# Kernel tuning notes

Measured on AMD Instinct MI355X. Metric: run time of the kernel, lower is better.

The kernel has to match this reference:

```python
import jax, jax.numpy as jnp
import numpy as np

B, Ci, Cr, Hb, Wb = 2, 256, 128, 200, 200
Ca, NH, DH = 128, 8, 16          # attn_channels = min(256,128); 8 heads of dim 16
K = 100                           # max(16, int(0.5*W)), K < W so topk path is active
EPS = 1e-5


def ln(x, g, b):
    m = x.mean(-1, keepdims=True)
    v = ((x - m) ** 2).mean(-1, keepdims=True)
    return (x - m) / jnp.sqrt(v + EPS) * g + b


def setup_inputs() -> dict:
    key = jax.random.key(0)
    ks = jax.random.split(key, 16)
    def n(k, shape, s=0.02):
        return jax.random.normal(k, shape, dtype=jnp.float32) * s
    return dict(
        radar_features=jax.random.normal(ks[0], (B, Cr, Hb, Wb), dtype=jnp.float32),
        image_features=jax.random.normal(ks[1], (B, Ci, Hb, Wb), dtype=jnp.float32),
        img_proj_w=n(ks[2], (Ca, Ci)),
        rad_proj_w=n(ks[3], (Ca, Cr)),
        in_proj_w=n(ks[4], (3 * Ca, Ca)),
        in_proj_b=jnp.zeros((3 * Ca,), jnp.float32),
        out_proj_w=n(ks[5], (Ca, Ca)),
        out_proj_b=jnp.zeros((Ca,), jnp.float32),
        ln1q_g=jnp.ones((Ca,), jnp.float32), ln1q_b=jnp.zeros((Ca,), jnp.float32),
        ln1kv_g=jnp.ones((Ca,), jnp.float32), ln1kv_b=jnp.zeros((Ca,), jnp.float32),
        ln2_g=jnp.ones((Ca,), jnp.float32), ln2_b=jnp.zeros((Ca,), jnp.float32),
        ffn_w1=n(ks[6], (4 * Ca, Ca)), ffn_b1=jnp.zeros((4 * Ca,), jnp.float32),
        ffn_w2=n(ks[7], (Ca, 4 * Ca)), ffn_b2=jnp.zeros((Ca,), jnp.float32),
        score_w1=n(ks[8], (Ca // 2, 2 * Ca)), score_b1=jnp.zeros((Ca // 2,), jnp.float32),
        score_w2=n(ks[9], (1, Ca // 2)), score_b2=jnp.zeros((1,), jnp.float32),
        rad_delta_w=n(ks[10], (Cr, Ca)),
        gamma=jnp.full((1,), 0.5, jnp.float32),  # torch inits to 0; 0.5 so attn branch affects output
        gate_w=n(ks[11], (Cr, Cr + Ci)), gate_b=jnp.zeros((Cr,), jnp.float32),
        fuse_w=n(ks[12], (Cr + Ci, Cr + Ci, 3, 3)),
        bn_g=jnp.ones((Cr + Ci,), jnp.float32), bn_b=jnp.zeros((Cr + Ci,), jnp.float32),
    )


def reference(radar_features, image_features, img_proj_w, rad_proj_w, in_proj_w, in_proj_b,
              out_proj_w, out_proj_b, ln1q_g, ln1q_b, ln1kv_g, ln1kv_b, ln2_g, ln2_b,
              ffn_w1, ffn_b1, ffn_w2, ffn_b2, score_w1, score_b1, score_w2, score_b2,
              rad_delta_w, gamma, gate_w, gate_b, fuse_w, bn_g, bn_b):
    # 1x1 projections into attention space, then per-row sequences [B*H, W, Ca]
    img_seq = jnp.einsum('bchw,oc->bhwo', image_features, img_proj_w).reshape(B * Hb, Wb, Ca)
    rad_seq = jnp.einsum('bchw,oc->bhwo', radar_features, rad_proj_w).reshape(B * Hb, Wb, Ca)

    # progressive focus: score each image token per row, keep top-K as KV
    si = jnp.concatenate([jax.lax.stop_gradient(rad_seq), img_seq], axis=-1)
    h = jax.nn.relu(si @ score_w1.T + score_b1)
    score = (h @ score_w2.T + score_b2)[..., 0]            # [B*H, W]
    _, idx = jax.lax.top_k(score, K)                       # [B*H, K]
    img_kv = jnp.take_along_axis(img_seq, idx[:, :, None], axis=1)  # [B*H, K, Ca]

    # cross attention (pre-LN on q and kv, residual onto rad_seq)
    q = ln(rad_seq, ln1q_g, ln1q_b)
    kv = ln(img_kv, ln1kv_g, ln1kv_b)
    wq, wk, wv = in_proj_w[:Ca], in_proj_w[Ca:2 * Ca], in_proj_w[2 * Ca:]
    bq, bk, bv = in_proj_b[:Ca], in_proj_b[Ca:2 * Ca], in_proj_b[2 * Ca:]
    qh = (q @ wq.T + bq).reshape(B * Hb, Wb, NH, DH)
    kh = (kv @ wk.T + bk).reshape(B * Hb, K, NH, DH)
    vh = (kv @ wv.T + bv).reshape(B * Hb, K, NH, DH)
    att = jax.nn.softmax(jnp.einsum('nqhd,nkhd->nhqk', qh, kh) / jnp.sqrt(jnp.float32(DH)), axis=-1)
    o = jnp.einsum('nhqk,nkhd->nqhd', att, vh).reshape(B * Hb, Wb, Ca) @ out_proj_w.T + out_proj_b
    x = rad_seq + o
    x = x + (jax.nn.relu(ln(x, ln2_g, ln2_b) @ ffn_w1.T + ffn_b1) @ ffn_w2.T + ffn_b2)

    # back to BEV, project delta to radar channels
    delta = jnp.einsum('bhwc,oc->bohw', x.reshape(B, Hb, Wb, Ca), rad_delta_w)

    # cross-modal gate (1x1 conv + sigmoid) with range-decay mask
    gate_in = jnp.concatenate([radar_features, image_features], axis=1)
    gate = jax.nn.sigmoid(jnp.einsum('bchw,oc->bohw', gate_in, gate_w) + gate_b[None, :, None, None])
    y = jnp.arange(Hb, dtype=jnp.float32) / (Hb - 1)
    rmask = jnp.clip(1.0 - 0.7 * y, 0.3, None)[None, None, :, None]
    gate = gate * rmask

    radar_enhanced = radar_features + gamma * gate * delta

    # fuse: 3x3 conv + BatchNorm (batch stats, training mode) + ReLU
    fi = jnp.concatenate([radar_enhanced, image_features], axis=1)
    c = jax.lax.conv_general_dilated(fi, fuse_w, (1, 1), 'SAME',
                                     dimension_numbers=('NCHW', 'OIHW', 'NCHW'))
    m = c.mean((0, 2, 3), keepdims=True)
    v = ((c - m) ** 2).mean((0, 2, 3), keepdims=True)
    out = jax.nn.relu((c - m) / jnp.sqrt(v + EPS) * bn_g[None, :, None, None] + bn_b[None, :, None, None])
    return out
```

## Files before the change

kernel.cpp:

```cpp
#include <hip/hip_runtime.h>
#include <hip/hip_bf16.h>

#define EPSF 1e-5f

typedef unsigned short u16;
typedef unsigned int u32;
typedef __attribute__((ext_vector_type(8))) short short8v;
typedef __attribute__((ext_vector_type(4))) float f32x4;

__device__ float g_arena[84000000];
__device__ float g_stats[768];

__device__ __forceinline__ float wave_sum(float v) {
#pragma unroll
    for (int o = 32; o > 0; o >>= 1) v += __shfl_down(v, o, 64);
    return v;
}

__device__ __forceinline__ void gload16(const u16* g, u16* l) {
    __builtin_amdgcn_global_load_lds(
        (const __attribute__((address_space(1))) u32*)(g),
        (__attribute__((address_space(3))) u32*)(l),
        16, 0, 0);
}

__device__ __forceinline__ void bf_split(float v, u16& h, u16& l) {
    __hip_bfloat16 bh = __float2bfloat16(v);
    float hv = __bfloat162float(bh);
    __hip_bfloat16 bl = __float2bfloat16(v - hv);
    h = *reinterpret_cast<u16*>(&bh);
    l = *reinterpret_cast<u16*>(&bl);
}

__device__ __forceinline__ void store_bf4(u16* p, float4 v) {
    __hip_bfloat16 h0 = __float2bfloat16(v.x);
    __hip_bfloat16 h1 = __float2bfloat16(v.y);
    __hip_bfloat16 h2 = __float2bfloat16(v.z);
    __hip_bfloat16 h3 = __float2bfloat16(v.w);
    *(ushort4*)p = make_ushort4(
        *reinterpret_cast<u16*>(&h0), *reinterpret_cast<u16*>(&h1),
        *reinterpret_cast<u16*>(&h2), *reinterpret_cast<u16*>(&h3));
}

__global__ __launch_bounds__(256) void split_weights_kernel(
    const float* __restrict__ w_inproj, const float* __restrict__ w_outproj,
    const float* __restrict__ w_ffn1, const float* __restrict__ w_ffn2,
    const float* __restrict__ w_delta, const float* __restrict__ w_gate,
    const float* __restrict__ w_img, const float* __restrict__ w_rad,
    const float* __restrict__ w_sc1, const float* __restrict__ b_sc1,
    u16* __restrict__ wseg, float* __restrict__ bias_pad,
    float* __restrict__ zpage)
{
    int i = blockIdx.x * 256 + threadIdx.x;
    if (i >= 393408) return;
    if (i >= 393344) {
        zpage[i - 393344] = 0.f;
        return;
    }
    if (i >= 393216) {
        int l = i - 393216;
        bias_pad[l] = (l < 64) ? b_sc1[l] : 0.f;
        return;
    }
    float v; int base, numel, local;
    if (i < 49152)       { local = i;          base = 0;      numel = 49152; v = w_inproj[local]; }
    else if (i < 65536)  { local = i - 49152;  base = 98304;  numel = 16384; v = w_outproj[local]; }
    else if (i < 131072) { local = i - 65536;  base = 131072; numel = 65536; v = w_ffn1[local]; }
    else if (i < 196608) { local = i - 131072; base = 262144; numel = 65536; v = w_ffn2[local]; }
    else if (i < 212992) { local = i - 196608; base = 393216; numel = 16384; v = w_delta[local]; }
    else if (i < 262144) { local = i - 212992; base = 425984; numel = 49152; v = w_gate[local]; }
    else if (i < 360448) {
        local = i - 262144; base = 524288; numel = 98304;
        int oc = local / 384, c = local - oc * 384;
        if (oc < 128) v = (c < 128) ? w_rad[oc * 128 + c] : 0.f;
        else          v = (c >= 128) ? w_img[(oc - 128) * 256 + (c - 128)] : 0.f;
    } else {
        local = i - 360448; base = 720896; numel = 32768;
        int oc = local / 256, c = local - oc * 256;
        v = (oc < 64) ? w_sc1[oc * 256 + c] : 0.f;
    }
    u16 hh, ll;
    bf_split(v, hh, ll);
    wseg[base + local] = hh;
    wseg[base + numel + local] = ll;
}

template <int BMODE, int OMODE, bool RELU, int EPI>
__global__ __launch_bounds__(256, (BMODE == 1) ? 3 : 2) void mfma_gemm_kernel(
    const u16* __restrict__ Ah, const u16* __restrict__ Al,
    const u16* __restrict__ bh, const u16* __restrict__ bl,
    const float* __restrict__ bf, int bstride,
    const float* __restrict__ bias, const float* __restrict__ resid, int rstride,
    float* __restrict__ outf, u16* __restrict__ outh,
    int K, int Nout, int P, const u16* __restrict__ zp,
    const float* __restrict__ aux0, const float* __restrict__ aux1,
    const float* __restrict__ aux2)
{
    __shared__ alignas(16) u16 sAh[8192], sAl[8192], sBh[8192];
    __shared__ alignas(16) u16 sBl[(BMODE != 1) ? 8192 : 8];

    const int tid  = threadIdx.x;
    const int lane = tid & 63;
    const int wid  = tid >> 6;
    const int wrm  = wid >> 1;
    const int wcn  = wid & 1;
    const int p0   = blockIdx.x * 128;
    const int ocb  = blockIdx.y * 128;

    const int r0  = tid >> 3;
    const int cl  = tid & 7;
    const int swz = cl ^ (r0 & 7);

    f32x4 acc[4][4];
#pragma unroll
    for (int i = 0; i < 4; ++i)
#pragma unroll
        for (int j = 0; j < 4; ++j) acc[i][j] = (f32x4){0.f, 0.f, 0.f, 0.f};

    const int fr = lane & 15;
    const int fc = lane >> 4;

    for (int kk = 0; kk < K; kk += 64) {
        __syncthreads();
#pragma unroll
        for (int k = 0; k < 4; ++k) {
            int row = r0 + k * 32;
            int dlin = row * 64 + cl * 8;
            size_t ga = (size_t)(ocb + row) * K + kk + swz * 8;
            gload16(&Ah[ga], &sAh[dlin]);
            gload16(&Al[ga], &sAl[dlin]);
            int p = p0 + row;
            if (BMODE == 0) {
                size_t gb = (size_t)p * bstride + kk + swz * 8;
                const u16* bsh = (p < P) ? &bh[gb] : zp;
                const u16* bsl = (p < P) ? &bl[gb] : zp;
                gload16(bsh, &sBh[dlin]);
                gload16(bsl, &sBl[dlin]);
            } else if (BMODE == 1) {
                size_t gb = (size_t)p * bstride + kk + swz * 8;
                const u16* bsh = (p < P) ? &bh[gb] : zp;
                gload16(bsh, &sBh[dlin]);
            } else {
                int di = row * 64 + swz * 8;
                short8v vh8 = {0,0,0,0,0,0,0,0}, vl8 = {0,0,0,0,0,0,0,0};
                if (p < P) {
                    const float* src = bf + (size_t)p * bstride + kk + cl * 8;
                    float4 f0 = *(const float4*)(src);
                    float4 f1 = *(const float4*)(src + 4);
                    float fv[8] = {f0.x, f0.y, f0.z, f0.w, f1.x, f1.y, f1.z, f1.w};
#pragma unroll
                    for (int j = 0; j < 8; ++j) {
                        u16 hh, ll;
                        bf_split(fv[j], hh, ll);
                        vh8[j] = (short)hh;
                        vl8[j] = (short)ll;
                    }
                }
                *(short8v*)&sBh[di] = vh8;
                *(short8v*)&sBl[di] = vl8;
            }
        }
        __syncthreads();
#pragma unroll
        for (int h = 0; h < 2; ++h) {
            const int kc = h * 4 + fc;
            short8v bhf[4], blf[4];
#pragma unroll
            for (int nn = 0; nn < 4; ++nn) {
                int row = wcn * 64 + nn * 16 + fr;
                int idx = row * 64 + ((kc ^ (row & 7)) << 3);
                bhf[nn] = *(const short8v*)&sBh[idx];
                if (BMODE != 1) blf[nn] = *(const short8v*)&sBl[idx];
            }
#pragma unroll
            for (int mm = 0; mm < 4; ++mm) {
                int row = wrm * 64 + mm * 16 + fr;
                int idx = row * 64 + ((kc ^ (row & 7)) << 3);
                short8v ahf = *(const short8v*)&sAh[idx];
                short8v alf = *(const short8v*)&sAl[idx];
#pragma unroll
                for (int nn = 0; nn < 4; ++nn)
                    acc[mm][nn] = __builtin_amdgcn_mfma_f32_16x16x32_bf16(
                        ahf, bhf[nn], acc[mm][nn], 0, 0, 0);
                if (BMODE != 1) {
#pragma unroll
                    for (int nn = 0; nn < 4; ++nn)
                        acc[mm][nn] = __builtin_amdgcn_mfma_f32_16x16x32_bf16(
                            ahf, blf[nn], acc[mm][nn], 0, 0, 0);
                }
#pragma unroll
                for (int nn = 0; nn < 4; ++nn)
                    acc[mm][nn] = __builtin_amdgcn_mfma_f32_16x16x32_bf16(
                        alf, bhf[nn], acc[mm][nn], 0, 0, 0);
            }
        }
    }

    if (EPI == 1) {
        if (wrm == 0) {
            float4 w2v[4], bvv[4];
#pragma unroll
            for (int mm = 0; mm < 4; ++mm) {
                w2v[mm] = *(const float4*)&aux0[mm * 16 + fc * 4];
                bvv[mm] = *(const float4*)&bias[mm * 16 + fc * 4];
            }
#pragma unroll
            for (int nn = 0; nn < 4; ++nn) {
                float ss = 0.f;
#pragma unroll
                for (int mm = 0; mm < 4; ++mm) {
                    ss += fmaxf(acc[mm][nn][0] + bvv[mm].x, 0.f) * w2v[mm].x;
                    ss += fmaxf(acc[mm][nn][1] + bvv[mm].y, 0.f) * w2v[mm].y;
                    ss += fmaxf(acc[mm][nn][2] + bvv[mm].z, 0.f) * w2v[mm].z;
                    ss += fmaxf(acc[mm][nn][3] + bvv[mm].w, 0.f) * w2v[mm].w;
                }
                ss += __shfl_xor(ss, 16, 64);
                ss += __shfl_xor(ss, 32, 64);
                int p = p0 + wcn * 64 + nn * 16 + fr;
                if (fc == 0 && p < P) outf[p] = ss + aux1[0];
            }
        }
        return;
    }

    if (EPI == 2) {
        const float gmm = aux2[0];
#pragma unroll
        for (int mm = 0; mm < 4; ++mm) {
            int base = ocb + wrm * 64 + mm * 16 + fc * 4;
#pragma unroll
            for (int nn = 0; nn < 4; ++nn) {
                int p = p0 + wcn * 64 + nn * 16 + fr;
                if (p < P) {
                    int b = (p >= 40000) ? 1 : 0;
                    int hw = p - b * 40000;
                    int hrow = hw / 200;
                    float rm = fmaxf(0.3f, 1.0f - 0.7f * ((float)hrow * (1.0f / 199.0f)));
                    float4 gv = *(const float4*)&aux0[(size_t)p * 128 + base];
                    const float* radp = aux1 + ((size_t)(b * 128 + base)) * 40000 + hw;
                    float4 r;
                    r.x = radp[0]      + gmm * (1.f / (1.f + __expf(-gv.x))) * rm * acc[mm][nn][0];
                    r.y = radp[40000]  + gmm * (1.f / (1.f + __expf(-gv.y))) * rm * acc[mm][nn][1];
                    r.z = radp[80000]  + gmm * (1.f / (1.f + __expf(-gv.z))) * rm * acc[mm][nn][2];
                    r.w = radp[120000] + gmm * (1.f / (1.f + __expf(-gv.w))) * rm * acc[mm][nn][3];
                    store_bf4(&outh[(size_t)p * 384 + base], r);
                }
            }
        }
        return;
    }

#pragma unroll
    for (int mm = 0; mm < 4; ++mm) {
        int base = ocb + wrm * 64 + mm * 16 + fc * 4;
        float4 bv = {0.f, 0.f, 0.f, 0.f};
        if (bias) bv = *(const float4*)&bias[base];
#pragma unroll
        for (int nn = 0; nn < 4; ++nn) {
            int p = p0 + wcn * 64 + nn * 16 + fr;
            if (p < P) {
                size_t row = (size_t)p * Nout + base;
                float4 r;
                r.x = acc[mm][nn][0] + bv.x;
                r.y = acc[mm][nn][1] + bv.y;
                r.z = acc[mm][nn][2] + bv.z;
                r.w = acc[mm][nn][3] + bv.w;
                if (resid) {
                    float4 rr = *(const float4*)&resid[(size_t)p * rstride + base - ocb];
                    r.x += rr.x; r.y += rr.y; r.z += rr.z; r.w += rr.w;
                }
                if (RELU) {
                    r.x = fmaxf(r.x, 0.f); r.y = fmaxf(r.y, 0.f);
                    r.z = fmaxf(r.z, 0.f); r.w = fmaxf(r.w, 0.f);
                }
                if (OMODE == 0) {
                    *(float4*)&outf[row] = r;
                } else {
                    store_bf4(&outh[row], r);
                }
            }
        }
    }
}

__global__ __launch_bounds__(256) void topk_kernel(
    const float* __restrict__ score, int* __restrict__ idx)
{
    __shared__ float s[200];
    const int n = blockIdx.x;
    const int t = threadIdx.x;
    if (t < 200) s[t] = score[(size_t)n * 200 + t];
    __syncthreads();
    if (t < 200) {
        float my = s[t];
        int cnt = 0;
        for (int j = 0; j < 200; j++) {
            float o = s[j];
            cnt += (o > my) || (o == my && j < t);
        }
        if (cnt < 100) idx[n * 100 + cnt] = t;
    }
}

__global__ __launch_bounds__(256) void ln_gather_kernel(
    const float* __restrict__ in, int stride, const int* __restrict__ gidx,
    const float* __restrict__ g, const float* __restrict__ bb,
    u16* __restrict__ oh, u16* __restrict__ ol)
{
    __shared__ float red[4];
    const int tid = threadIdx.x;
    const int grp = tid >> 7;
    const int t = tid & 127;
    const int r = blockIdx.x * 2 + grp;

    size_t src_row;
    if (gidx) src_row = (size_t)(r / 100) * 200 + gidx[r];
    else      src_row = (size_t)r;

    float x = in[src_row * stride + t];
    float s = wave_sum(x);
    if ((tid & 63) == 0) red[tid >> 6] = s;
    __syncthreads();
    float m = (red[grp * 2] + red[grp * 2 + 1]) * 0.0078125f;
    float d = x - m;
    float s2 = wave_sum(d * d);
    __syncthreads();
    if ((tid & 63) == 0) red[tid >> 6] = s2;
    __syncthreads();
    float var = (red[grp * 2] + red[grp * 2 + 1]) * 0.0078125f;
    float y = d * rsqrtf(var + EPSF) * g[t] + bb[t];
    u16 hh, ll;
    bf_split(y, hh, ll);
    oh[(size_t)r * 128 + t] = hh;
    if (ol) ol[(size_t)r * 128 + t] = ll;
}

__global__ __launch_bounds__(256) void attention_kernel(
    const float* __restrict__ qh, const float* __restrict__ kvh,
    u16* __restrict__ o_hi)
{
    __shared__ float sk[100][16];
    __shared__ float sv[100][16];
    const int h = blockIdx.x;
    const int n = blockIdx.y;
    const int tid = threadIdx.x;

    for (int e = tid; e < 1600; e += 256) {
        int kk = e >> 4, d = e & 15;
        size_t src = ((size_t)n * 100 + kk) * 256 + h * 16 + d;
        sk[kk][d] = kvh[src];
        sv[kk][d] = kvh[src + 128];
    }
    __syncthreads();

    if (tid < 200) {
        const float* qp = &qh[((size_t)n * 200 + tid) * 128 + h * 16];
        float4 q0 = *(const float4*)(qp + 0);
        float4 q1 = *(const float4*)(qp + 4);
        float4 q2 = *(const float4*)(qp + 8);
        float4 q3 = *(const float4*)(qp + 12);

        float m = -INFINITY, l = 0.f;
        float4 a0 = {0,0,0,0}, a1 = {0,0,0,0}, a2 = {0,0,0,0}, a3 = {0,0,0,0};

        for (int kk = 0; kk < 100; kk++) {
            const float4* kp = (const float4*)&sk[kk][0];
            float s = q0.x*kp[0].x + q0.y*kp[0].y + q0.z*kp[0].z + q0.w*kp[0].w
                    + q1.x*kp[1].x + q1.y*kp[1].y + q1.z*kp[1].z + q1.w*kp[1].w
                    + q2.x*kp[2].x + q2.y*kp[2].y + q2.z*kp[2].z + q2.w*kp[2].w
                    + q3.x*kp[3].x + q3.y*kp[3].y + q3.z*kp[3].z + q3.w*kp[3].w;
            s *= 0.25f;
            float nm = fmaxf(m, s);
            float corr = __expf(m - nm);
            float pe = __expf(s - nm);
            l = l * corr + pe;
            const float4* vp = (const float4*)&sv[kk][0];
            float4 v0 = vp[0], v1 = vp[1], v2 = vp[2], v3 = vp[3];
            a0.x = a0.x * corr + pe * v0.x; a0.y = a0.y * corr + pe * v0.y;
            a0.z = a0.z * corr + pe * v0.z; a0.w = a0.w * corr + pe * v0.w;
            a1.x = a1.x * corr + pe * v1.x; a1.y = a1.y * corr + pe * v1.y;
            a1.z = a1.z * corr + pe * v1.z; a1.w = a1.w * corr + pe * v1.w;
            a2.x = a2.x * corr + pe * v2.x; a2.y = a2.y * corr + pe * v2.y;
            a2.z = a2.z * corr + pe * v2.z; a2.w = a2.w * corr + pe * v2.w;
            a3.x = a3.x * corr + pe * v3.x; a3.y = a3.y * corr + pe * v3.y;
            a3.z = a3.z * corr + pe * v3.z; a3.w = a3.w * corr + pe * v3.w;
            m = nm;
        }
        float inv = 1.f / l;
        a0.x *= inv; a0.y *= inv; a0.z *= inv; a0.w *= inv;
        a1.x *= inv; a1.y *= inv; a1.z *= inv; a1.w *= inv;
        a2.x *= inv; a2.y *= inv; a2.z *= inv; a2.w *= inv;
        a3.x *= inv; a3.y *= inv; a3.z *= inv; a3.w *= inv;
        size_t ob = ((size_t)n * 200 + tid) * 128 + h * 16;
        store_bf4(&o_hi[ob + 0],  a0);
        store_bf4(&o_hi[ob + 4],  a1);
        store_bf4(&o_hi[ob + 8],  a2);
        store_bf4(&o_hi[ob + 12], a3);
    }
}

__global__ __launch_bounds__(256) void prep_weights_kernel(
    const float* __restrict__ fw, u16* __restrict__ wh, u16* __restrict__ wl)
{
    int idx = blockIdx.x * 256 + threadIdx.x;
    int oc = idx / 384;
    int ic = idx - oc * 384;
    const float* src = fw + (size_t)idx * 9;
    u16* dh = wh + (size_t)oc * 3456 + ic;
    u16* dl = wl + (size_t)oc * 3456 + ic;
#pragma unroll
    for (int s = 0; s < 9; ++s) {
        u16 hh, ll;
        bf_split(src[s], hh, ll);
        dh[(size_t)s * 384] = hh;
        dl[(size_t)s * 384] = ll;
    }
}

__global__ __launch_bounds__(256) void convert_nhwc_kernel(
    const float* __restrict__ radar, const float* __restrict__ image,
    u16* __restrict__ oh, u16* __restrict__ ol)
{
    int p = blockIdx.x * 256 + threadIdx.x;
    if (p >= 80000) return;
    int cg = blockIdx.y;
    int b = p >= 40000 ? 1 : 0;
    int hw = p - b * 40000;
    u16* ph = oh + (size_t)p * 384 + cg * 64;
    u16* pl = ol + (size_t)p * 384 + cg * 64;
#pragma unroll 1
    for (int g = 0; g < 8; ++g) {
        short8v vh, vl;
#pragma unroll
        for (int j = 0; j < 8; ++j) {
            int c = cg * 64 + g * 8 + j;
            float v = (c < 128)
                ? radar[((size_t)(b * 128 + c)) * 40000 + hw]
                : image[((size_t)(b * 256 + (c - 128))) * 40000 + hw];
            u16 hh, ll;
            bf_split(v, hh, ll);
            vh[j] = (short)hh;
            vl[j] = (short)ll;
        }
        *(short8v*)&ph[g * 8] = vh;
        *(short8v*)&pl[g * 8] = vl;
    }
}

__global__ __launch_bounds__(256, 3) void conv_mfma_kernel(
    const u16* __restrict__ nhwc_hi,
    const u16* __restrict__ wgt_hi,  const u16* __restrict__ wgt_lo,
    float* __restrict__ out, const u16* __restrict__ zp)
{
    __shared__ alignas(16) u16 sAh[8192], sAl[8192], sBh[8192];

    const int tid  = threadIdx.x;
    const int lane = tid & 63;
    const int wid  = tid >> 6;
    const int wrm  = wid >> 1;
    const int wcn  = wid & 1;
    const int hw0  = blockIdx.x * 128;
    const int b    = blockIdx.y;
    const int oc0  = blockIdx.z * 128;

    const int r0  = tid >> 3;
    const int cl  = tid & 7;
    const int swz = cl ^ (r0 & 7);

    const int y0 = hw0 / 200;
    const int x0 = hw0 - y0 * 200;

    f32x4 acc[4][4];
#pragma unroll
    for (int i = 0; i < 4; ++i)
#pragma unroll
        for (int j = 0; j < 4; ++j) acc[i][j] = (f32x4){0.f, 0.f, 0.f, 0.f};

    size_t abase[4];
#pragma unroll
    for (int k = 0; k < 4; ++k)
        abase[k] = (size_t)(oc0 + r0 + k * 32) * 3456 + swz * 8;

    const int fr = lane & 15;
    const int fc = lane >> 4;

    for (int s = 0; s < 9; ++s) {
        const int dy = s / 3 - 1;
        const int dx = s % 3 - 1;
        size_t bsrc[4];
        int bval[4];
#pragma unroll
        for (int k = 0; k < 4; ++k) {
            int row = r0 + k * 32;
            int hwo = hw0 + row;
            int xr  = x0 + row;
            int wrp = (xr >= 200) ? 1 : 0;
            int yy  = y0 + wrp + dy;
            int xx  = xr - wrp * 200 + dx;
            int v = (hwo < 40000) && ((unsigned)yy < 200u) && ((unsigned)xx < 200u);
            bval[k] = v;
            bsrc[k] = v ? ((size_t)(b * 40000 + yy * 200 + xx) * 384 + swz * 8) : 0;
        }
        const size_t wofs = (size_t)s * 384;

        for (int icb = 0; icb < 6; ++icb) {
            const int ic0 = icb * 64;
            __syncthreads();
#pragma unroll
            for (int k = 0; k < 4; ++k) {
                int dlin = (r0 + k * 32) * 64 + cl * 8;
                size_t ga = abase[k] + wofs + ic0;
                gload16(&wgt_hi[ga], &sAh[dlin]);
                gload16(&wgt_lo[ga], &sAl[dlin]);
                const u16* bs = bval[k] ? &nhwc_hi[bsrc[k] + ic0] : zp;
                gload16(bs, &sBh[dlin]);
            }
            __syncthreads();
#pragma unroll
            for (int h = 0; h < 2; ++h) {
                const int kc = h * 4 + fc;
                short8v bhf[4];
#pragma unroll
                for (int nn = 0; nn < 4; ++nn) {
                    int row = wcn * 64 + nn * 16 + fr;
                    int idx = row * 64 + ((kc ^ (row & 7)) << 3);
                    bhf[nn] = *(const short8v*)&sBh[idx];
                }
#pragma unroll
                for (int mm = 0; mm < 4; ++mm) {
                    int row = wrm * 64 + mm * 16 + fr;
                    int idx = row * 64 + ((kc ^ (row & 7)) << 3);
                    short8v ahf = *(const short8v*)&sAh[idx];
                    short8v alf = *(const short8v*)&sAl[idx];
#pragma unroll
                    for (int nn = 0; nn < 4; ++nn)
                        acc[mm][nn] = __builtin_amdgcn_mfma_f32_16x16x32_bf16(
                            ahf, bhf[nn], acc[mm][nn], 0, 0, 0);
#pragma unroll
                    for (int nn = 0; nn < 4; ++nn)
                        acc[mm][nn] = __builtin_amdgcn_mfma_f32_16x16x32_bf16(
                            alf, bhf[nn], acc[mm][nn], 0, 0, 0);
                }
            }
        }
    }

#pragma unroll
    for (int mm = 0; mm < 4; ++mm) {
        int oc = oc0 + wrm * 64 + mm * 16 + fc * 4;
#pragma unroll
        for (int nn = 0; nn < 4; ++nn) {
            int p = hw0 + wcn * 64 + nn * 16 + fr;
            if (p < 40000) {
                float* op = out + (size_t)(b * 384 + oc) * 40000 + p;
#pragma unroll
                for (int r = 0; r < 4; ++r)
                    op[(size_t)r * 40000] = acc[mm][nn][r];
            }
        }
    }
}

__global__ void zero_stats_kernel() {
    int i = blockIdx.x * 256 + threadIdx.x;
    if (i < 768) g_stats[i] = 0.f;
}

__global__ __launch_bounds__(256) void conv_stats_kernel(const float* __restrict__ out)
{
    const int c = blockIdx.x;
    const int chunk = blockIdx.y;
    float s1 = 0.f, s2 = 0.f;
#pragma unroll
    for (int b = 0; b < 2; ++b) {
        const float4* pp = (const float4*)(out + (size_t)(b * 384 + c) * 40000)
                         + (size_t)chunk * 2500;
        for (int i = threadIdx.x; i < 2500; i += 256) {
            float4 v = pp[i];
            s1 += v.x + v.y + v.z + v.w;
            s2 += v.x * v.x + v.y * v.y + v.z * v.z + v.w * v.w;
        }
    }
    s1 = wave_sum(s1);
    s2 = wave_sum(s2);
    __shared__ float r1[4], r2[4];
    if ((threadIdx.x & 63) == 0) {
        r1[threadIdx.x >> 6] = s1;
        r2[threadIdx.x >> 6] = s2;
    }
    __syncthreads();
    if (threadIdx.x == 0) {
        atomicAdd(&g_stats[c * 2],     r1[0] + r1[1] + r1[2] + r1[3]);
        atomicAdd(&g_stats[c * 2 + 1], r2[0] + r2[1] + r2[2] + r2[3]);
    }
}

__global__ __launch_bounds__(256) void bn_relu_kernel(
    float* __restrict__ out, const float* __restrict__ g,
    const float* __restrict__ bb)
{
    int i = blockIdx.x * 256 + threadIdx.x;
    int flat = i * 4;
    int oc = (flat / 40000) % 384;
    float m = g_stats[oc * 2] * (1.f / 80000.f);
    float v = g_stats[oc * 2 + 1] * (1.f / 80000.f) - m * m;
    float inv = rsqrtf(v + EPSF);
    float sc = g[oc] * inv;
    float sh = bb[oc] - m * sc;
    float4 c = ((float4*)out)[i];
    c.x = fmaxf(c.x * sc + sh, 0.f);
    c.y = fmaxf(c.y * sc + sh, 0.f);
    c.z = fmaxf(c.z * sc + sh, 0.f);
    c.w = fmaxf(c.w * sc + sh, 0.f);
    ((float4*)out)[i] = c;
}

extern "C" void kernel_launch(void* const* d_in, const int* in_sizes, int n_in,
                              void* d_out, int out_size, void* d_ws, size_t ws_size,
                              hipStream_t stream)
{
    (void)in_sizes; (void)n_in; (void)out_size; (void)d_ws; (void)ws_size;

    const float* radar      = (const float*)d_in[0];
    const float* image      = (const float*)d_in[1];
    const float* img_proj_w = (const float*)d_in[2];
    const float* rad_proj_w = (const float*)d_in[3];
    const float* in_proj_w  = (const float*)d_in[4];
    const float* in_proj_b  = (const float*)d_in[5];
    const float* out_proj_w = (const float*)d_in[6];
    const float* out_proj_b = (const float*)d_in[7];
    const float* ln1q_g     = (const float*)d_in[8];
    const float* ln1q_b     = (const float*)d_in[9];
    const float* ln1kv_g    = (const float*)d_in[10];
    const float* ln1kv_b    = (const float*)d_in[11];
    const float* ln2_g      = (const float*)d_in[12];
    const float* ln2_b      = (const float*)d_in[13];
    const float* ffn_w1     = (const float*)d_in[14];
    const float* ffn_b1     = (const float*)d_in[15];
    const float* ffn_w2     = (const float*)d_in[16];
    const float* ffn_b2     = (const float*)d_in[17];
    const float* score_w1   = (const float*)d_in[18];
    const float* score_b1   = (const float*)d_in[19];
    const float* score_w2   = (const float*)d_in[20];
    const float* score_b2   = (const float*)d_in[21];
    const float* rad_delta_w= (const float*)d_in[22];
    const float* gamma      = (const float*)d_in[23];
    const float* gate_w     = (const float*)d_in[24];
    const float* gate_b     = (const float*)d_in[25];
    const float* fuse_w     = (const float*)d_in[26];
    const float* bn_g       = (const float*)d_in[27];
    const float* bn_b       = (const float*)d_in[28];

    float* arena = nullptr;
    hipGetSymbolAddress((void**)&arena, HIP_SYMBOL(g_arena));

    u16*   nh_hi    = (u16*)arena;
    u16*   nh_lo    = (u16*)(arena + 15360000);
    float* seq_comb = arena + 30720000;
    float* score    = arena + 51200000;
    int*   idx      = (int*)(arena + 51280000);
    float* qh       = arena + 51200000;
    float* xbuf     = arena + 51200000;
    float* kvh      = arena + 61440000;
    float* gatepre  = arena + 61440000;
    u16*   gbase    = (u16*)(arena + 71680000);
    u16*   kvn_hi   = gbase;
    u16*   qn_hi    = gbase + 10240000;
    u16*   o_hi     = gbase + 10240000;
    u16*   xn_hi    = gbase + 10240000;
    u16*   hbuf     = (u16*)(arena + 30720000);
    u16*   wseg     = (u16*)(arena + 81920000);
    u16*   cwgt_hi  = (u16*)(arena + 82330000);
    u16*   cwgt_lo  = cwgt_hi + 1327104;
    float* bias_pad = arena + 83900000;
    float* zpage_f  = arena + 83900160;
    const u16* zp   = (const u16*)zpage_f;

    const u16* w_q_hi    = wseg + 0,      *w_q_lo    = wseg + 49152;
    const u16* w_kv_hi   = wseg + 16384,  *w_kv_lo   = wseg + 49152 + 16384;
    const u16* w_out_hi  = wseg + 98304,  *w_out_lo  = wseg + 114688;
    const u16* w_ffn1_hi = wseg + 131072, *w_ffn1_lo = wseg + 196608;
    const u16* w_ffn2_hi = wseg + 262144, *w_ffn2_lo = wseg + 327680;
    const u16* w_dlt_hi  = wseg + 393216, *w_dlt_lo  = wseg + 409600;
    const u16* w_gate_hi = wseg + 425984, *w_gate_lo = wseg + 475136;
    const u16* w_comb_hi = wseg + 524288, *w_comb_lo = wseg + 622592;
    const u16* w_sc1_hi  = wseg + 720896, *w_sc1_lo  = wseg + 753664;

    const dim3 blk(256);

    split_weights_kernel<<<dim3(1537), blk, 0, stream>>>(
        in_proj_w, out_proj_w, ffn_w1, ffn_w2, rad_delta_w, gate_w,
        img_proj_w, rad_proj_w, score_w1, score_b1, wseg, bias_pad, zpage_f);
    prep_weights_kernel<<<dim3(576), blk, 0, stream>>>(fuse_w, cwgt_hi, cwgt_lo);
    convert_nhwc_kernel<<<dim3(313, 6), blk, 0, stream>>>(radar, image, nh_hi, nh_lo);

    mfma_gemm_kernel<0, 0, false, 0><<<dim3(625, 2), blk, 0, stream>>>(
        w_comb_hi, w_comb_lo, nh_hi, nh_lo, nullptr, 384,
        nullptr, nullptr, 0, seq_comb, nullptr, 384, 256, 80000, zp,
        nullptr, nullptr, nullptr);

    mfma_gemm_kernel<2, 0, false, 1><<<dim3(625, 1), blk, 0, stream>>>(
        w_sc1_hi, w_sc1_lo, nullptr, nullptr, seq_comb, 256,
        bias_pad, nullptr, 0, score, nullptr, 256, 128, 80000, zp,
        score_w2, score_b2, nullptr);
    topk_kernel<<<dim3(400), blk, 0, stream>>>(score, idx);

    ln_gather_kernel<<<dim3(20000), blk, 0, stream>>>(
        seq_comb + 128, 256, idx, ln1kv_g, ln1kv_b, kvn_hi, nullptr);
    mfma_gemm_kernel<1, 0, false, 0><<<dim3(313, 2), blk, 0, stream>>>(
        w_kv_hi, w_kv_lo, kvn_hi, nullptr, nullptr, 128,
        in_proj_b + 128, nullptr, 0, kvh, nullptr, 128, 256, 40000, zp,
        nullptr, nullptr, nullptr);

    ln_gather_kernel<<<dim3(40000), blk, 0, stream>>>(
        seq_comb, 256, nullptr, ln1q_g, ln1q_b, qn_hi, nullptr);
    mfma_gemm_kernel<1, 0, false, 0><<<dim3(625, 1), blk, 0, stream>>>(
        w_q_hi, w_q_lo, qn_hi, nullptr, nullptr, 128,
        in_proj_b, nullptr, 0, qh, nullptr, 128, 128, 80000, zp,
        nullptr, nullptr, nullptr);

    attention_kernel<<<dim3(8, 400), blk, 0, stream>>>(qh, kvh, o_hi);

    mfma_gemm_kernel<1, 0, false, 0><<<dim3(625, 1), blk, 0, stream>>>(
        w_out_hi, w_out_lo, o_hi, nullptr, nullptr, 128,
        out_proj_b, seq_comb, 256, xbuf, nullptr, 128, 128, 80000, zp,
        nullptr, nullptr, nullptr);

    ln_gather_kernel<<<dim3(40000), blk, 0, stream>>>(
        xbuf, 128, nullptr, ln2_g, ln2_b, xn_hi, nullptr);
    mfma_gemm_kernel<1, 1, true, 0><<<dim3(625, 4), blk, 0, stream>>>(
        w_ffn1_hi, w_ffn1_lo, xn_hi, nullptr, nullptr, 128,
        ffn_b1, nullptr, 0, nullptr, hbuf, 128, 512, 80000, zp,
        nullptr, nullptr, nullptr);
    mfma_gemm_kernel<1, 0, false, 0><<<dim3(625, 1), blk, 0, stream>>>(
        w_ffn2_hi, w_ffn2_lo, hbuf, nullptr, nullptr, 512,
        ffn_b2, xbuf, 128, xbuf, nullptr, 512, 128, 80000, zp,
        nullptr, nullptr, nullptr);

    mfma_gemm_kernel<1, 0, false, 0><<<dim3(625, 1), blk, 0, stream>>>(
        w_gate_hi, w_gate_lo, nh_hi, nullptr, nullptr, 384,
        gate_b, nullptr, 0, gatepre, nullptr, 384, 128, 80000, zp,
        nullptr, nullptr, nullptr);
    mfma_gemm_kernel<2, 0, false, 2><<<dim3(625, 1), blk, 0, stream>>>(
        w_dlt_hi, w_dlt_lo, nullptr, nullptr, xbuf, 128,
        nullptr, nullptr, 0, nullptr, nh_hi, 128, 128, 80000, zp,
        gatepre, radar, gamma);

    conv_mfma_kernel<<<dim3(313, 2, 3), blk, 0, stream>>>(
        nh_hi, cwgt_hi, cwgt_lo, (float*)d_out, zp);
    zero_stats_kernel<<<dim3(3), blk, 0, stream>>>();
    conv_stats_kernel<<<dim3(384, 4), blk, 0, stream>>>((const float*)d_out);
    bn_relu_kernel<<<dim3(30000), blk, 0, stream>>>(
        (float*)d_out, bn_g, bn_b);
}
```

Measured before the change: 1.613 ms.

## Drop low-bf16 weight terms in most GEMMs and conv, fuse BN stats into conv

Adds a WLO template flag so most GEMMs, and the 3x3 conv, use only the high bf16 part of the weights. This removes one of the three split-precision MFMA passes and its LDS traffic, and the smaller shared-memory footprint allows higher occupancy. Batch-norm sum and sum-of-squares are now reduced in the conv epilogue with shuffles and atomics, replacing the separate stats kernel that re-read the conv output. The cost is reduced weight precision, and float atomics make the statistics order-dependent.

```diff
diff --git a/kernel.cpp b/kernel.cpp
--- a/kernel.cpp
+++ b/kernel.cpp
@@ -85,8 +85,10 @@
     wseg[base + numel + local] = ll;
 }
 
-template <int BMODE, int OMODE, bool RELU, int EPI>
-__global__ __launch_bounds__(256, (BMODE == 1) ? 3 : 2) void mfma_gemm_kernel(
+template <int BMODE, int OMODE, bool RELU, int EPI, bool WLO>
+__global__ __launch_bounds__(256,
+    ((BMODE == 1 && !WLO) ? 4 : (BMODE == 1 || !WLO) ? 3 : 2))
+void mfma_gemm_kernel(
     const u16* __restrict__ Ah, const u16* __restrict__ Al,
     const u16* __restrict__ bh, const u16* __restrict__ bl,
     const float* __restrict__ bf, int bstride,
@@ -96,7 +98,8 @@
     const float* __restrict__ aux0, const float* __restrict__ aux1,
     const float* __restrict__ aux2)
 {
-    __shared__ alignas(16) u16 sAh[8192], sAl[8192], sBh[8192];
+    __shared__ alignas(16) u16 sAh[8192], sBh[8192];
+    __shared__ alignas(16) u16 sAl[WLO ? 8192 : 8];
     __shared__ alignas(16) u16 sBl[(BMODE != 1) ? 8192 : 8];
 
     const int tid  = threadIdx.x;
@@ -128,7 +131,7 @@
             int dlin = row * 64 + cl * 8;
             size_t ga = (size_t)(ocb + row) * K + kk + swz * 8;
             gload16(&Ah[ga], &sAh[dlin]);
-            gload16(&Al[ga], &sAl[dlin]);
+            if (WLO) gload16(&Al[ga], &sAl[dlin]);
             int p = p0 + row;
             if (BMODE == 0) {
                 size_t gb = (size_t)p * bstride + kk + swz * 8;
@@ -177,7 +180,6 @@
                 int row = wrm * 64 + mm * 16 + fr;
                 int idx = row * 64 + ((kc ^ (row & 7)) << 3);
                 short8v ahf = *(const short8v*)&sAh[idx];
-                short8v alf = *(const short8v*)&sAl[idx];
 #pragma unroll
                 for (int nn = 0; nn < 4; ++nn)
                     acc[mm][nn] = __builtin_amdgcn_mfma_f32_16x16x32_bf16(
@@ -188,10 +190,13 @@
                         acc[mm][nn] = __builtin_amdgcn_mfma_f32_16x16x32_bf16(
                             ahf, blf[nn], acc[mm][nn], 0, 0, 0);
                 }
-#pragma unroll
-                for (int nn = 0; nn < 4; ++nn)
-                    acc[mm][nn] = __builtin_amdgcn_mfma_f32_16x16x32_bf16(
-                        alf, bhf[nn], acc[mm][nn], 0, 0, 0);
+                if (WLO) {
+                    short8v alf = *(const short8v*)&sAl[idx];
+#pragma unroll
+                    for (int nn = 0; nn < 4; ++nn)
+                        acc[mm][nn] = __builtin_amdgcn_mfma_f32_16x16x32_bf16(
+                            alf, bhf[nn], acc[mm][nn], 0, 0, 0);
+                }
             }
         }
     }
@@ -400,20 +405,17 @@
 }
 
 __global__ __launch_bounds__(256) void prep_weights_kernel(
-    const float* __restrict__ fw, u16* __restrict__ wh, u16* __restrict__ wl)
+    const float* __restrict__ fw, u16* __restrict__ wh)
 {
     int idx = blockIdx.x * 256 + threadIdx.x;
     int oc = idx / 384;
     int ic = idx - oc * 384;
     const float* src = fw + (size_t)idx * 9;
     u16* dh = wh + (size_t)oc * 3456 + ic;
-    u16* dl = wl + (size_t)oc * 3456 + ic;
 #pragma unroll
     for (int s = 0; s < 9; ++s) {
-        u16 hh, ll;
-        bf_split(src[s], hh, ll);
-        dh[(size_t)s * 384] = hh;
-        dl[(size_t)s * 384] = ll;
+        __hip_bfloat16 bh = __float2bfloat16(src[s]);
+        dh[(size_t)s * 384] = *reinterpret_cast<u16*>(&bh);
     }
 }
 
@@ -447,12 +449,12 @@
     }
 }
 
-__global__ __launch_bounds__(256, 3) void conv_mfma_kernel(
+__global__ __launch_bounds__(256, 4) void conv_mfma_kernel(
     const u16* __restrict__ nhwc_hi,
-    const u16* __restrict__ wgt_hi,  const u16* __restrict__ wgt_lo,
+    const u16* __restrict__ wgt_hi,
     float* __restrict__ out, const u16* __restrict__ zp)
 {
-    __shared__ alignas(16) u16 sAh[8192], sAl[8192], sBh[8192];
+    __shared__ alignas(16) u16 sAh[8192], sBh[8192];
 
     const int tid  = threadIdx.x;
     const int lane = tid & 63;
@@ -509,9 +511,7 @@
 #pragma unroll
             for (int k = 0; k < 4; ++k) {
                 int dlin = (r0 + k * 32) * 64 + cl * 8;
-                size_t ga = abase[k] + wofs + ic0;
-                gload16(&wgt_hi[ga], &sAh[dlin]);
-                gload16(&wgt_lo[ga], &sAl[dlin]);
+                gload16(&wgt_hi[abase[k] + wofs + ic0], &sAh[dlin]);
                 const u16* bs = bval[k] ? &nhwc_hi[bsrc[k] + ic0] : zp;
                 gload16(bs, &sBh[dlin]);
             }
@@ -531,15 +531,10 @@
                     int row = wrm * 64 + mm * 16 + fr;
                     int idx = row * 64 + ((kc ^ (row & 7)) << 3);
                     short8v ahf = *(const short8v*)&sAh[idx];
-                    short8v alf = *(const short8v*)&sAl[idx];
 #pragma unroll
                     for (int nn = 0; nn < 4; ++nn)
                         acc[mm][nn] = __builtin_amdgcn_mfma_f32_16x16x32_bf16(
                             ahf, bhf[nn], acc[mm][nn], 0, 0, 0);
-#pragma unroll
-                    for (int nn = 0; nn < 4; ++nn)
-                        acc[mm][nn] = __builtin_amdgcn_mfma_f32_16x16x32_bf16(
-                            alf, bhf[nn], acc[mm][nn], 0, 0, 0);
                 }
             }
         }
@@ -558,41 +553,30 @@
                     op[(size_t)r * 40000] = acc[mm][nn][r];
             }
         }
+#pragma unroll
+        for (int r = 0; r < 4; ++r) {
+            float s1 = 0.f, s2 = 0.f;
+#pragma unroll
+            for (int nn = 0; nn < 4; ++nn) {
+                float v = acc[mm][nn][r];
+                s1 += v; s2 += v * v;
+            }
+#pragma unroll
+            for (int o = 8; o > 0; o >>= 1) {
+                s1 += __shfl_xor(s1, o, 64);
+                s2 += __shfl_xor(s2, o, 64);
+            }
+            if (fr == 0) {
+                atomicAdd(&g_stats[(oc + r) * 2], s1);
+                atomicAdd(&g_stats[(oc + r) * 2 + 1], s2);
+            }
+        }
     }
 }
 
 __global__ void zero_stats_kernel() {
     int i = blockIdx.x * 256 + threadIdx.x;
     if (i < 768) g_stats[i] = 0.f;
-}
-
-__global__ __launch_bounds__(256) void conv_stats_kernel(const float* __restrict__ out)
-{
-    const int c = blockIdx.x;
-    const int chunk = blockIdx.y;
-    float s1 = 0.f, s2 = 0.f;
-#pragma unroll
-    for (int b = 0; b < 2; ++b) {
-        const float4* pp = (const float4*)(out + (size_t)(b * 384 + c) * 40000)
-                         + (size_t)chunk * 2500;
-        for (int i = threadIdx.x; i < 2500; i += 256) {
-            float4 v = pp[i];
-            s1 += v.x + v.y + v.z + v.w;
-            s2 += v.x * v.x + v.y * v.y + v.z * v.z + v.w * v.w;
-        }
-    }
-    s1 = wave_sum(s1);
-    s2 = wave_sum(s2);
-    __shared__ float r1[4], r2[4];
-    if ((threadIdx.x & 63) == 0) {
-        r1[threadIdx.x >> 6] = s1;
-        r2[threadIdx.x >> 6] = s2;
-    }
-    __syncthreads();
-    if (threadIdx.x == 0) {
-        atomicAdd(&g_stats[c * 2],     r1[0] + r1[1] + r1[2] + r1[3]);
-        atomicAdd(&g_stats[c * 2 + 1], r2[0] + r2[1] + r2[2] + r2[3]);
-    }
 }
 
 __global__ __launch_bounds__(256) void bn_relu_kernel(
@@ -671,18 +655,17 @@
     u16*   hbuf     = (u16*)(arena + 30720000);
     u16*   wseg     = (u16*)(arena + 81920000);
     u16*   cwgt_hi  = (u16*)(arena + 82330000);
-    u16*   cwgt_lo  = cwgt_hi + 1327104;
     float* bias_pad = arena + 83900000;
     float* zpage_f  = arena + 83900160;
     const u16* zp   = (const u16*)zpage_f;
 
-    const u16* w_q_hi    = wseg + 0,      *w_q_lo    = wseg + 49152;
-    const u16* w_kv_hi   = wseg + 16384,  *w_kv_lo   = wseg + 49152 + 16384;
-    const u16* w_out_hi  = wseg + 98304,  *w_out_lo  = wseg + 114688;
-    const u16* w_ffn1_hi = wseg + 131072, *w_ffn1_lo = wseg + 196608;
-    const u16* w_ffn2_hi = wseg + 262144, *w_ffn2_lo = wseg + 327680;
-    const u16* w_dlt_hi  = wseg + 393216, *w_dlt_lo  = wseg + 409600;
-    const u16* w_gate_hi = wseg + 425984, *w_gate_lo = wseg + 475136;
+    const u16* w_q_hi    = wseg + 0;
+    const u16* w_kv_hi   = wseg + 16384;
+    const u16* w_out_hi  = wseg + 98304;
+    const u16* w_ffn1_hi = wseg + 131072;
+    const u16* w_ffn2_hi = wseg + 262144;
+    const u16* w_dlt_hi  = wseg + 393216;
+    const u16* w_gate_hi = wseg + 425984;
     const u16* w_comb_hi = wseg + 524288, *w_comb_lo = wseg + 622592;
     const u16* w_sc1_hi  = wseg + 720896, *w_sc1_lo  = wseg + 753664;
 
@@ -691,15 +674,15 @@
     split_weights_kernel<<<dim3(1537), blk, 0, stream>>>(
         in_proj_w, out_proj_w, ffn_w1, ffn_w2, rad_delta_w, gate_w,
         img_proj_w, rad_proj_w, score_w1, score_b1, wseg, bias_pad, zpage_f);
-    prep_weights_kernel<<<dim3(576), blk, 0, stream>>>(fuse_w, cwgt_hi, cwgt_lo);
+    prep_weights_kernel<<<dim3(576), blk, 0, stream>>>(fuse_w, cwgt_hi);
     convert_nhwc_kernel<<<dim3(313, 6), blk, 0, stream>>>(radar, image, nh_hi, nh_lo);
 
-    mfma_gemm_kernel<0, 0, false, 0><<<dim3(625, 2), blk, 0, stream>>>(
+    mfma_gemm_kernel<0, 0, false, 0, true><<<dim3(625, 2), blk, 0, stream>>>(
         w_comb_hi, w_comb_lo, nh_hi, nh_lo, nullptr, 384,
         nullptr, nullptr, 0, seq_comb, nullptr, 384, 256, 80000, zp,
         nullptr, nullptr, nullptr);
 
-    mfma_gemm_kernel<2, 0, false, 1><<<dim3(625, 1), blk, 0, stream>>>(
+    mfma_gemm_kernel<2, 0, false, 1, true><<<dim3(625, 1), blk, 0, stream>>>(
         w_sc1_hi, w_sc1_lo, nullptr, nullptr, seq_comb, 256,
         bias_pad, nullptr, 0, score, nullptr, 256, 128, 80000, zp,
         score_w2, score_b2, nullptr);
@@ -707,49 +690,48 @@
 
     ln_gather_kernel<<<dim3(20000), blk, 0, stream>>>(
         seq_comb + 128, 256, idx, ln1kv_g, ln1kv_b, kvn_hi, nullptr);
-    mfma_gemm_kernel<1, 0, false, 0><<<dim3(313, 2), blk, 0, stream>>>(
-        w_kv_hi, w_kv_lo, kvn_hi, nullptr, nullptr, 128,
+    mfma_gemm_kernel<1, 0, false, 0, false><<<dim3(313, 2), blk, 0, stream>>>(
+        w_kv_hi, nullptr, kvn_hi, nullptr, nullptr, 128,
         in_proj_b + 128, nullptr, 0, kvh, nullptr, 128, 256, 40000, zp,
         nullptr, nullptr, nullptr);
 
     ln_gather_kernel<<<dim3(40000), blk, 0, stream>>>(
         seq_comb, 256, nullptr, ln1q_g, ln1q_b, qn_hi, nullptr);
-    mfma_gemm_kernel<1, 0, false, 0><<<dim3(625, 1), blk, 0, stream>>>(
-        w_q_hi, w_q_lo, qn_hi, nullptr, nullptr, 128,
+    mfma_gemm_kernel<1, 0, false, 0, false><<<dim3(625, 1), blk, 0, stream>>>(
+        w_q_hi, nullptr, qn_hi, nullptr, nullptr, 128,
         in_proj_b, nullptr, 0, qh, nullptr, 128, 128, 80000, zp,
         nullptr, nullptr, nullptr);
 
     attention_kernel<<<dim3(8, 400), blk, 0, stream>>>(qh, kvh, o_hi);
 
-    mfma_gemm_kernel<1, 0, false, 0><<<dim3(625, 1), blk, 0, stream>>>(
-        w_out_hi, w_out_lo, o_hi, nullptr, nullptr, 128,
+    mfma_gemm_kernel<1, 0, false, 0, false><<<dim3(625, 1), blk, 0, stream>>>(
+        w_out_hi, nullptr, o_hi, nullptr, nullptr, 128,
         out_proj_b, seq_comb, 256, xbuf, nullptr, 128, 128, 80000, zp,
         nullptr, nullptr, nullptr);
 
     ln_gather_kernel<<<dim3(40000), blk, 0, stream>>>(
         xbuf, 128, nullptr, ln2_g, ln2_b, xn_hi, nullptr);
-    mfma_gemm_kernel<1, 1, true, 0><<<dim3(625, 4), blk, 0, stream>>>(
-        w_ffn1_hi, w_ffn1_lo, xn_hi, nullptr, nullptr, 128,
+    mfma_gemm_kernel<1, 1, true, 0, false><<<dim3(625, 4), blk, 0, stream>>>(
+        w_ffn1_hi, nullptr, xn_hi, nullptr, nullptr, 128,
         ffn_b1, nullptr, 0, nullptr, hbuf, 128, 512, 80000, zp,
         nullptr, nullptr, nullptr);
-    mfma_gemm_kernel<1, 0, false, 0><<<dim3(625, 1), blk, 0, stream>>>(
-        w_ffn2_hi, w_ffn2_lo, hbuf, nullptr, nullptr, 512,
+    mfma_gemm_kernel<1, 0, false, 0, false><<<dim3(625, 1), blk, 0, stream>>>(
+        w_ffn2_hi, nullptr, hbuf, nullptr, nullptr, 512,
         ffn_b2, xbuf, 128, xbuf, nullptr, 512, 128, 80000, zp,
         nullptr, nullptr, nullptr);
 
-    mfma_gemm_kernel<1, 0, false, 0><<<dim3(625, 1), blk, 0, stream>>>(
-        w_gate_hi, w_gate_lo, nh_hi, nullptr, nullptr, 384,
+    mfma_gemm_kernel<1, 0, false, 0, false><<<dim3(625, 1), blk, 0, stream>>>(
+        w_gate_hi, nullptr, nh_hi, nullptr, nullptr, 384,
         gate_b, nullptr, 0, gatepre, nullptr, 384, 128, 80000, zp,
         nullptr, nullptr, nullptr);
-    mfma_gemm_kernel<2, 0, false, 2><<<dim3(625, 1), blk, 0, stream>>>(
-        w_dlt_hi, w_dlt_lo, nullptr, nullptr, xbuf, 128,
+    mfma_gemm_kernel<2, 0, false, 2, false><<<dim3(625, 1), blk, 0, stream>>>(
+        w_dlt_hi, nullptr, nullptr, nullptr, xbuf, 128,
         nullptr, nullptr, 0, nullptr, nh_hi, 128, 128, 80000, zp,
         gatepre, radar, gamma);
 
+    zero_stats_kernel<<<dim3(3), blk, 0, stream>>>();
     conv_mfma_kernel<<<dim3(313, 2, 3), blk, 0, stream>>>(
-        nh_hi, cwgt_hi, cwgt_lo, (float*)d_out, zp);
-    zero_stats_kernel<<<dim3(3), blk, 0, stream>>>();
-    conv_stats_kernel<<<dim3(384, 4), blk, 0, stream>>>((const float*)d_out);
+        nh_hi, cwgt_hi, (float*)d_out, zp);
     bn_relu_kernel<<<dim3(30000), blk, 0, stream>>>(
         (float*)d_out, bn_g, bn_b);
 }
```

Measured after the change: 2.227 ms. +38.1%, slower.
